# Kernel tuning notes

Hardware: AMD Instinct MI355X
Metric: run time of the kernel (lower is better)

Reference implementation:

```python
import jax, jax.numpy as jnp
import numpy as np

B, T, D, U, W = 8, 1024, 1024, 1024, 2  # batch, seq_len, input_dim, units, window_size


def setup_inputs() -> dict:
    key = jax.random.key(0)
    k1, k2 = jax.random.split(key)
    x = jax.random.normal(k1, (B, T, D), dtype=jnp.float32)
    # keras 'uniform' initializer: U(-0.05, 0.05); kernel squeezed from (W,1,D,3U) to (W,D,3U)
    kernel = jax.random.uniform(k2, (W, D, 3 * U), dtype=jnp.float32, minval=-0.05, maxval=0.05)
    bias = jnp.zeros((3 * U,), dtype=jnp.float32)  # 'zero' initializer
    return {"x": x, "kernel": kernel, "bias": bias}


def reference(x, kernel, bias):
    Wk, Din, U3 = kernel.shape
    Un = U3 // 3
    Tn = x.shape[1]
    # causal temporal padding (window_size-1 on the left), then valid windowed conv
    xp = jnp.pad(x, ((0, 0), (Wk - 1, 0), (0, 0)))
    # gates[b,t] = sum_k xp[b,t+k] @ kernel[k] + bias  -> [B,T,3U]
    gates = sum(jnp.einsum('btd,du->btu', xp[:, k:k + Tn], kernel[k]) for k in range(Wk)) + bias
    z = jnp.tanh(gates[..., :Un])
    f = jax.nn.sigmoid(gates[..., Un:2 * Un])
    o = jax.nn.sigmoid(gates[..., 2 * Un:])

    def step(h, zfo):
        zt, ft, ot = zfo
        h_new = ot * (ft * h + (1.0 - ft) * zt)
        return h_new, h_new

    h0 = jnp.zeros((x.shape[0], Un), dtype=x.dtype)
    _, hs = jax.lax.scan(step, h0, (z.swapaxes(0, 1), f.swapaxes(0, 1), o.swapaxes(0, 1)))
    return hs.swapaxes(0, 1)  # [B,T,U] (return_sequences=True)
```

## Files before the change

kernel.cpp:

```cpp
#include <hip/hip_runtime.h>
#include <hip/hip_bf16.h>

typedef __bf16 bf16x8 __attribute__((ext_vector_type(8)));
typedef float f32x4 __attribute__((ext_vector_type(4)));

#define GLOBAL_AS(p) ((const __attribute__((address_space(1))) void*)(p))
#define LDS_AS(p)    ((__attribute__((address_space(3))) void*)(p))

static __device__ __forceinline__ unsigned short f2bf(float f) {
    union { float f; unsigned u; } v; v.f = f;
    unsigned r = v.u + 0x7FFFu + ((v.u >> 16) & 1u);
    return (unsigned short)(r >> 16);
}

__global__ void prep_xb(const float* __restrict__ x, unsigned short* __restrict__ xb2) {
    const int bid = blockIdx.x;
    const int c = threadIdx.x * 4;
    if (bid < 8192) {
        const int dst = bid + (bid >> 10) + 1;
        float4 v = *reinterpret_cast<const float4*>(x + (size_t)bid * 1024 + c);
        ushort4 b = make_ushort4(f2bf(v.x), f2bf(v.y), f2bf(v.z), f2bf(v.w));
        *reinterpret_cast<ushort4*>(xb2 + (size_t)dst * 1024 + c) = b;
    } else {
        const int zr = (bid - 8192) * 1025;
        *reinterpret_cast<ushort4*>(xb2 + (size_t)zr * 1024 + c) = make_ushort4(0, 0, 0, 0);
    }
}

__global__ void prep_kt(const float* __restrict__ K, unsigned short* __restrict__ KT) {
    __shared__ float tile[64][65];
    const int bi = blockIdx.x;
    const int bj = blockIdx.y;
    const int tx = threadIdx.x & 63;
    const int ty = threadIdx.x >> 6;

#pragma unroll
    for (int i = 0; i < 16; ++i) {
        int r = ty * 16 + i;
        tile[r][tx] = K[(size_t)(bi * 64 + r) * 3072 + bj * 64 + tx];
    }
    __syncthreads();
#pragma unroll
    for (int i = 0; i < 16; ++i) {
        int r = ty * 16 + i;
        KT[(size_t)(bj * 64 + r) * 2048 + bi * 64 + tx] = f2bf(tile[tx][r]);
    }
}

__global__ __launch_bounds__(256, 2)
void gemm_gates(const unsigned short* __restrict__ xb2,
                const unsigned short* __restrict__ BT,
                const float* __restrict__ bias,
                _Float16* __restrict__ G) {
    __shared__ __align__(16) unsigned short As[128 * 64];
    __shared__ __align__(16) unsigned short Bs[128 * 64];

    const int tid  = threadIdx.x;
    const int lane = tid & 63;
    const int wid  = tid >> 6;
    const int wr   = wid >> 1, wc = wid & 1;
    const int m0   = blockIdx.y * 128;
    const int n0   = blockIdx.x * 128;

    f32x4 acc[4][4] = {};

    const int sr = lane >> 3;
    const int sc = lane & 7;

    const unsigned short* srcA[4];
    const unsigned short* srcB[4];
#pragma unroll
    for (int i = 0; i < 4; ++i) {
        const int r  = wid * 32 + i * 8 + sr;
        const int cc = sc ^ (r & 7);
        const int m  = m0 + r;
        srcA[i] = xb2 + (size_t)(m + (m >> 10)) * 1024 + cc * 8;
        srcB[i] = BT  + (size_t)(n0 + r) * 2048 + cc * 8;
    }

    for (int kt = 0; kt < 32; ++kt) {
        const int kb = kt * 64;
#pragma unroll
        for (int i = 0; i < 4; ++i) {
            const int r0 = wid * 32 + i * 8;
            __builtin_amdgcn_global_load_lds(GLOBAL_AS(srcA[i] + kb), LDS_AS(As + r0 * 64), 16, 0, 0);
            __builtin_amdgcn_global_load_lds(GLOBAL_AS(srcB[i] + kb), LDS_AS(Bs + r0 * 64), 16, 0, 0);
        }
        __syncthreads();

#pragma unroll
        for (int ks = 0; ks < 2; ++ks) {
            bf16x8 af[4], bg[4];
#pragma unroll
            for (int m = 0; m < 4; ++m) {
                const int row = wr * 64 + m * 16 + (lane & 15);
                const int c   = ks * 4 + (lane >> 4);
                const int p   = c ^ (row & 7);
                af[m] = *reinterpret_cast<const bf16x8*>(As + row * 64 + p * 8);
            }
#pragma unroll
            for (int n = 0; n < 4; ++n) {
                const int row = wc * 64 + n * 16 + (lane & 15);
                const int c   = ks * 4 + (lane >> 4);
                const int p   = c ^ (row & 7);
                bg[n] = *reinterpret_cast<const bf16x8*>(Bs + row * 64 + p * 8);
            }
#pragma unroll
            for (int m = 0; m < 4; ++m)
#pragma unroll
                for (int n = 0; n < 4; ++n)
                    acc[m][n] = __builtin_amdgcn_mfma_f32_16x16x32_bf16(af[m], bg[n], acc[m][n], 0, 0, 0);
        }
        __syncthreads();
    }

    const int rgn = n0 >> 10;
#pragma unroll
    for (int m = 0; m < 4; ++m) {
#pragma unroll
        for (int n = 0; n < 4; ++n) {
            const int col = n0 + wc * 64 + n * 16 + (lane & 15);
            const float bv = bias[col];
#pragma unroll
            for (int v = 0; v < 4; ++v) {
                const int row = m0 + wr * 64 + m * 16 + ((lane >> 4) * 4) + v;
                const float g = acc[m][n][v] + bv;
                float val;
                if (rgn == 0) {
                    float s = 1.0f / (1.0f + __expf(-2.0f * g));
                    val = 2.0f * s - 1.0f;
                } else {
                    val = 1.0f / (1.0f + __expf(-g));
                }
                G[(size_t)row * 3072 + col] = (_Float16)val;
            }
        }
    }
}

__global__ void scan_pass1(const _Float16* __restrict__ G, float2* __restrict__ AB) {
    const int bid = blockIdx.x;
    const int b   = bid / 28;
    const int r   = bid % 28;
    const int c   = r >> 2;
    const int ug  = r & 3;
    const int u   = ug * 256 + threadIdx.x;
    const _Float16* g = G + (size_t)(b * 1024 + c * 128) * 3072 + u;
    float A = 1.f, Bv = 0.f;
#pragma unroll 8
    for (int i = 0; i < 128; ++i) {
        const float zv = (float)g[(size_t)i * 3072];
        const float fv = (float)g[(size_t)i * 3072 + 1024];
        const float ov = (float)g[(size_t)i * 3072 + 2048];
        const float a  = ov * fv;
        const float bb = ov * (1.f - fv) * zv;
        A  = a * A;
        Bv = a * Bv + bb;
    }
    AB[(size_t)(b * 8 + c) * 1024 + u] = make_float2(A, Bv);
}

__global__ void scan_pass23(const _Float16* __restrict__ G, const float2* __restrict__ AB,
                            float* __restrict__ out) {
    const int bid = blockIdx.x;
    const int b   = bid >> 7;
    const int r   = bid & 127;
    const int c   = r >> 4;
    const int ug  = r & 15;
    const int u   = ug * 64 + threadIdx.x;

    float h = 0.f;
    for (int j = 0; j < c; ++j) {
        float2 p = AB[(size_t)(b * 8 + j) * 1024 + u];
        h = p.x * h + p.y;
    }
    const _Float16* g = G + (size_t)(b * 1024 + c * 128) * 3072 + u;
    float* o = out + (size_t)(b * 1024 + c * 128) * 1024 + u;
#pragma unroll 8
    for (int i = 0; i < 128; ++i) {
        const float zv = (float)g[(size_t)i * 3072];
        const float fv = (float)g[(size_t)i * 3072 + 1024];
        const float ov = (float)g[(size_t)i * 3072 + 2048];
        h = ov * (fv * h + (1.f - fv) * zv);
        o[(size_t)i * 1024] = h;
    }
}

extern "C" void kernel_launch(void* const* d_in, const int* in_sizes, int n_in,
                              void* d_out, int out_size, void* d_ws, size_t ws_size,
                              hipStream_t stream) {
    const float* x    = (const float*)d_in[0];
    const float* kern = (const float*)d_in[1];
    const float* bias = (const float*)d_in[2];
    float* out = (float*)d_out;

    char* ws = (char*)d_ws;
    unsigned short* xb2 = (unsigned short*)ws;
    unsigned short* KT  = (unsigned short*)(ws + 16793600);
    _Float16* G         = (_Float16*)(ws + 29376512);
    float2* AB          = (float2*)(ws + 79708160);

    prep_xb<<<dim3(8200), dim3(256), 0, stream>>>(x, xb2);
    prep_kt<<<dim3(32, 48), dim3(256), 0, stream>>>(kern, KT);
    gemm_gates<<<dim3(24, 64), dim3(256), 0, stream>>>(xb2, KT, bias, G);
    scan_pass1<<<dim3(224), dim3(256), 0, stream>>>(G, AB);
    scan_pass23<<<dim3(1024), dim3(64), 0, stream>>>(G, AB, out);
}
```

Baseline: 152.2 us.

## Double-buffer LDS tiles in gates GEMM to overlap global loads with MFMA

The gates GEMM now keeps two LDS buffers per operand and prefetches the tile two steps ahead. It waits with explicit vmcnt counters, reads all fragments into registers, and then issues the next global-to-LDS loads before running the MFMAs. It also uses inline ds_read_b128 and setprio around the MFMA block. The goal is to hide global memory latency behind compute, at the cost of doubled LDS (64KB per block). That extra LDS may limit occupancy, and the hand-counted waitcnt values are fragile.

```diff
diff --git a/kernel.cpp b/kernel.cpp
--- a/kernel.cpp
+++ b/kernel.cpp
@@ -6,6 +6,10 @@
 
 #define GLOBAL_AS(p) ((const __attribute__((address_space(1))) void*)(p))
 #define LDS_AS(p)    ((__attribute__((address_space(3))) void*)(p))
+#define BAR()        asm volatile("s_barrier" ::: "memory")
+
+typedef __attribute__((address_space(3))) const unsigned short* lds_sp;
+#define DSREAD(dst, ptr) asm volatile("ds_read_b128 %0, %1" : "=v"(dst) : "v"((lds_sp)(ptr)))
 
 static __device__ __forceinline__ unsigned short f2bf(float f) {
     union { float f; unsigned u; } v; v.f = f;
@@ -52,8 +56,8 @@
                 const unsigned short* __restrict__ BT,
                 const float* __restrict__ bias,
                 _Float16* __restrict__ G) {
-    __shared__ __align__(16) unsigned short As[128 * 64];
-    __shared__ __align__(16) unsigned short Bs[128 * 64];
+    __shared__ __align__(16) unsigned short As[2 * 128 * 64];
+    __shared__ __align__(16) unsigned short Bs[2 * 128 * 64];
 
     const int tid  = threadIdx.x;
     const int lane = tid & 63;
@@ -61,6 +65,7 @@
     const int wr   = wid >> 1, wc = wid & 1;
     const int m0   = blockIdx.y * 128;
     const int n0   = blockIdx.x * 128;
+    const int l15  = lane & 15, l16 = lane >> 4, l7 = lane & 7;
 
     f32x4 acc[4][4] = {};
 
@@ -78,40 +83,64 @@
         srcB[i] = BT  + (size_t)(n0 + r) * 2048 + cc * 8;
     }
 
-    for (int kt = 0; kt < 32; ++kt) {
+    auto stage = [&](int kt, int buf) {
         const int kb = kt * 64;
 #pragma unroll
         for (int i = 0; i < 4; ++i) {
             const int r0 = wid * 32 + i * 8;
-            __builtin_amdgcn_global_load_lds(GLOBAL_AS(srcA[i] + kb), LDS_AS(As + r0 * 64), 16, 0, 0);
-            __builtin_amdgcn_global_load_lds(GLOBAL_AS(srcB[i] + kb), LDS_AS(Bs + r0 * 64), 16, 0, 0);
+            __builtin_amdgcn_global_load_lds(GLOBAL_AS(srcA[i] + kb),
+                LDS_AS(As + buf * 8192 + r0 * 64), 16, 0, 0);
+            __builtin_amdgcn_global_load_lds(GLOBAL_AS(srcB[i] + kb),
+                LDS_AS(Bs + buf * 8192 + r0 * 64), 16, 0, 0);
         }
-        __syncthreads();
-
-#pragma unroll
-        for (int ks = 0; ks < 2; ++ks) {
-            bf16x8 af[4], bg[4];
-#pragma unroll
-            for (int m = 0; m < 4; ++m) {
-                const int row = wr * 64 + m * 16 + (lane & 15);
-                const int c   = ks * 4 + (lane >> 4);
-                const int p   = c ^ (row & 7);
-                af[m] = *reinterpret_cast<const bf16x8*>(As + row * 64 + p * 8);
+    };
+
+    stage(0, 0);
+    stage(1, 1);
+
+    auto do_iter = [&](int t, int buf) {
+        if (t < 31) { asm volatile("s_waitcnt vmcnt(8)" ::: "memory"); }
+        else        { asm volatile("s_waitcnt vmcnt(0)" ::: "memory"); }
+        BAR();
+
+        bf16x8 af[4][2], bg[4][2];
+#pragma unroll
+        for (int m = 0; m < 4; ++m)
+#pragma unroll
+            for (int ks = 0; ks < 2; ++ks) {
+                const int row = wr * 64 + m * 16 + l15;
+                const int p   = (ks * 4 + l16) ^ l7;
+                DSREAD(af[m][ks], As + buf * 8192 + row * 64 + p * 8);
             }
 #pragma unroll
-            for (int n = 0; n < 4; ++n) {
-                const int row = wc * 64 + n * 16 + (lane & 15);
-                const int c   = ks * 4 + (lane >> 4);
-                const int p   = c ^ (row & 7);
-                bg[n] = *reinterpret_cast<const bf16x8*>(Bs + row * 64 + p * 8);
+        for (int n = 0; n < 4; ++n)
+#pragma unroll
+            for (int ks = 0; ks < 2; ++ks) {
+                const int row = wc * 64 + n * 16 + l15;
+                const int p   = (ks * 4 + l16) ^ l7;
+                DSREAD(bg[n][ks], Bs + buf * 8192 + row * 64 + p * 8);
             }
-#pragma unroll
-            for (int m = 0; m < 4; ++m)
-#pragma unroll
-                for (int n = 0; n < 4; ++n)
-                    acc[m][n] = __builtin_amdgcn_mfma_f32_16x16x32_bf16(af[m], bg[n], acc[m][n], 0, 0, 0);
-        }
-        __syncthreads();
+        asm volatile("s_waitcnt lgkmcnt(0)" ::: "memory");
+        __builtin_amdgcn_sched_barrier(0);
+        BAR();
+
+        if (t < 30) stage(t + 2, buf);
+
+        __builtin_amdgcn_s_setprio(1);
+#pragma unroll
+        for (int m = 0; m < 4; ++m)
+#pragma unroll
+            for (int n = 0; n < 4; ++n)
+#pragma unroll
+                for (int ks = 0; ks < 2; ++ks)
+                    acc[m][n] = __builtin_amdgcn_mfma_f32_16x16x32_bf16(
+                        af[m][ks], bg[n][ks], acc[m][n], 0, 0, 0);
+        __builtin_amdgcn_s_setprio(0);
+    };
+
+    for (int tt = 0; tt < 16; ++tt) {
+        do_iter(tt * 2, 0);
+        do_iter(tt * 2 + 1, 1);
     }
 
     const int rgn = n0 >> 10;
@@ -119,11 +148,11 @@
     for (int m = 0; m < 4; ++m) {
 #pragma unroll
         for (int n = 0; n < 4; ++n) {
-            const int col = n0 + wc * 64 + n * 16 + (lane & 15);
+            const int col = n0 + wc * 64 + n * 16 + l15;
             const float bv = bias[col];
 #pragma unroll
             for (int v = 0; v < 4; ++v) {
-                const int row = m0 + wr * 64 + m * 16 + ((lane >> 4) * 4) + v;
+                const int row = m0 + wr * 64 + m * 16 + l16 * 4 + v;
                 const float g = acc[m][n][v] + bv;
                 float val;
                 if (rgn == 0) {
```

Result: no change. 151.5 us (-0.4%).
